# Optimization experiments

Measured on AMD Instinct MI355X. Metric: run time of the kernel, lower is better.

The kernel has to match this reference:

```python
import jax, jax.numpy as jnp
import numpy as np

N_LORAS = 8   # number of adapters (experts)
RANK = 16     # rank per adapter; rmoe = N_LORAS * RANK = 128
TEMP = 1.0    # self.T


def setup_inputs() -> dict:
    key = jax.random.key(0)
    ks = jax.random.split(key, 7)
    B, S, D_IN, D_OUT = 4, 2048, 4096, 4096
    RMOE = N_LORAS * RANK
    x = jax.random.normal(ks[0], (B, S, D_IN), dtype=jnp.float32)
    base_w = jax.random.normal(ks[1], (D_OUT, D_IN), dtype=jnp.float32) / np.sqrt(D_IN)
    base_b = jax.random.normal(ks[2], (D_OUT,), dtype=jnp.float32) * 0.01
    # nn.init.normal_(lora_A.weight, std=1/r); lora_B zero-init in torch, use small random here
    lora_A = jax.random.normal(ks[3], (RMOE, D_IN), dtype=jnp.float32) / RANK
    lora_B = jax.random.normal(ks[4], (D_OUT, RMOE), dtype=jnp.float32) * 0.02
    router_w = jax.random.normal(ks[5], (N_LORAS, D_IN), dtype=jnp.float32) / np.sqrt(D_IN)
    # scaling[name] = lora_alpha / sqrt(r) per adapter (use_rslora)
    scalings = jnp.full((N_LORAS,), 32.0 / np.sqrt(RANK), dtype=jnp.float32)
    return {"x": x, "base_w": base_w, "base_b": base_b, "lora_A": lora_A,
            "lora_B": lora_B, "router_w": router_w, "scalings": scalings, "top_k": 2}


def reference(x, base_w, base_b, lora_A, lora_B, router_w, scalings, top_k):
    # Base dense layer: y = x W^T + b
    base_out = jnp.einsum('bsd,od->bso', x, base_w) + base_b

    # Router: per-token logits over adapters, top-k, softmax over selected
    logits = jnp.einsum('bsd,ed->bse', x, router_w) / TEMP          # [B,S,E]
    topv, topi = jax.lax.top_k(logits, top_k)                        # [B,S,K]
    gate_k = jax.nn.softmax(topv, axis=-1)                           # [B,S,K]
    # dense per-expert gate: scatter top-k weights back to E slots
    gate_e = jnp.sum(jax.nn.one_hot(topi, N_LORAS, dtype=gate_k.dtype)
                     * gate_k[..., None], axis=-2)                   # [B,S,E]

    # Fused LoRA: h = x A^T over the concatenated rank dim, mask ranks by gate*scaling
    h = jnp.einsum('bsd,rd->bsr', x, lora_A)                         # [B,S,RMOE]
    rank_w = jnp.repeat(gate_e * scalings, RANK, axis=-1)            # [B,S,RMOE]
    lora_out = jnp.einsum('bsr,or->bso', h * rank_w, lora_B)         # [B,S,O]

    return base_out + lora_out
```

## Files before the change

### kernel.cpp

```cpp
#include <hip/hip_runtime.h>
#include <cstdint>

typedef unsigned short u16;
typedef float  f32x4 __attribute__((ext_vector_type(4)));
typedef short  s16x4 __attribute__((ext_vector_type(4)));
typedef short  s16x8 __attribute__((ext_vector_type(8)));

#define D_IN  4096
#define D_OUT 4096
#define RMOE  128
#define KAUG  4224
#define NTOK  8192

__device__ __forceinline__ u16 f2bf(float f) {
    unsigned u = __builtin_bit_cast(unsigned, f);
    unsigned r = u + 0x7fffu + ((u >> 16) & 1u);
    return (u16)(r >> 16);
}

__device__ __forceinline__ void gload16(const void* g, void* l) {
    __builtin_amdgcn_global_load_lds(
        (const __attribute__((address_space(1))) void*)g,
        (__attribute__((address_space(3))) void*)l, 16, 0, 0);
}

__global__ __launch_bounds__(256)
void xconv_router_kernel(const float* __restrict__ x, const float* __restrict__ rw,
                         const float* __restrict__ scal,
                         u16* __restrict__ Xaug, float* __restrict__ gates) {
    int wave = threadIdx.x >> 6, lane = threadIdx.x & 63;
    int t = blockIdx.x * 4 + wave;
    const float4* xp = (const float4*)(x + (long)t * D_IN);
    u16* xa = Xaug + (long)t * KAUG;
    float acc[8];
#pragma unroll
    for (int e = 0; e < 8; ++e) acc[e] = 0.f;
#pragma unroll 4
    for (int i = 0; i < 16; ++i) {
        float4 xv = xp[i * 64 + lane];
        s16x4 o;
        o[0] = (short)f2bf(xv.x); o[1] = (short)f2bf(xv.y);
        o[2] = (short)f2bf(xv.z); o[3] = (short)f2bf(xv.w);
        *(s16x4*)(xa + (i * 64 + lane) * 4) = o;
#pragma unroll
        for (int e = 0; e < 8; ++e) {
            float4 wv = ((const float4*)(rw + (long)e * D_IN))[i * 64 + lane];
            acc[e] += xv.x * wv.x + xv.y * wv.y + xv.z * wv.z + xv.w * wv.w;
        }
    }
#pragma unroll
    for (int e = 0; e < 8; ++e) {
#pragma unroll
        for (int off = 32; off > 0; off >>= 1)
            acc[e] += __shfl_xor(acc[e], off, 64);
    }
    if (lane == 0) {
        int i1 = 0; float v1 = acc[0];
#pragma unroll
        for (int e = 1; e < 8; ++e) if (acc[e] > v1) { v1 = acc[e]; i1 = e; }
        int i2 = -1; float v2 = -3.4e38f;
#pragma unroll
        for (int e = 0; e < 8; ++e) if (e != i1 && acc[e] > v2) { v2 = acc[e]; i2 = e; }
        float g1 = 1.f / (1.f + expf(v2 - v1));
        float g2 = 1.f - g1;
        float* gp = gates + (long)t * 8;
#pragma unroll
        for (int e = 0; e < 8; ++e)
            gp[e] = (e == i1) ? g1 * scal[e] : ((e == i2) ? g2 * scal[e] : 0.f);
    }
}

__global__ __launch_bounds__(256)
void convert_rest_kernel(const float* __restrict__ bw,
                         const float* __restrict__ lA, const float* __restrict__ lB,
                         u16* __restrict__ Waug, u16* __restrict__ A16) {
    const long nw = (long)D_OUT * D_IN / 8;
    const long nb = (long)D_OUT * RMOE / 8;
    long tid = (long)blockIdx.x * 256 + threadIdx.x;
    const float* src; u16* dst;
    if (tid < nw) {
        long e = tid * 8; long row = e >> 12; long col = e & 4095;
        src = bw + e; dst = Waug + row * KAUG + col;
    } else if (tid < nw + nb) {
        long e = (tid - nw) * 8; long row = e >> 7; long col = e & 127;
        src = lB + e; dst = Waug + row * KAUG + D_IN + col;
    } else {
        long e = (tid - nw - nb) * 8;
        src = lA + e; dst = A16 + e;
    }
    float4 a = ((const float4*)src)[0];
    float4 b = ((const float4*)src)[1];
    s16x8 o;
    o[0] = (short)f2bf(a.x); o[1] = (short)f2bf(a.y);
    o[2] = (short)f2bf(a.z); o[3] = (short)f2bf(a.w);
    o[4] = (short)f2bf(b.x); o[5] = (short)f2bf(b.y);
    o[6] = (short)f2bf(b.z); o[7] = (short)f2bf(b.w);
    *(s16x8*)dst = o;
}

__global__ __launch_bounds__(256)
void lora_h_kernel(u16* __restrict__ Xaug, const u16* __restrict__ A16,
                   const float* __restrict__ gates) {
    __shared__ u16 sX[64 * 32];
    __shared__ u16 sW[64 * 32];
    int tid = threadIdx.x, wave = tid >> 6, lane = tid & 63;
    int bm = blockIdx.x >> 1, bn = blockIdx.x & 1;
    long m0 = (long)bm * 64; int n0 = bn * 64;
    int wr = wave >> 1, wc = wave & 1;
    int c = wave * 64 + lane, row = c >> 2, oct = c & 3;
    const u16* gx = Xaug + (m0 + row) * KAUG + oct * 8;
    const u16* gw = A16 + (long)(n0 + row) * D_IN + oct * 8;
    u16* lx = sX + wave * 512;
    u16* lw = sW + wave * 512;
    int cl = lane & 15, kh = lane >> 4;
    int aoff[2], boff[2];
#pragma unroll
    for (int i = 0; i < 2; ++i) {
        aoff[i] = (wr * 32 + i * 16 + cl) * 32 + kh * 8;
        boff[i] = (wc * 32 + i * 16 + cl) * 32 + kh * 8;
    }
    f32x4 acc[2][2];
#pragma unroll
    for (int i = 0; i < 2; ++i)
#pragma unroll
        for (int j = 0; j < 2; ++j) acc[i][j] = (f32x4){0.f, 0.f, 0.f, 0.f};
    for (int kt = 0; kt < 128; ++kt) {
        __syncthreads();
        gload16(gx, lx); gload16(gw, lw);
        gx += 32; gw += 32;
        __syncthreads();
        s16x8 a[2], b[2];
#pragma unroll
        for (int i = 0; i < 2; ++i) {
            a[i] = *(const s16x8*)&sX[aoff[i]];
            b[i] = *(const s16x8*)&sW[boff[i]];
        }
#pragma unroll
        for (int mi = 0; mi < 2; ++mi)
#pragma unroll
            for (int ni = 0; ni < 2; ++ni)
                acc[mi][ni] = __builtin_amdgcn_mfma_f32_16x16x32_bf16(
                    a[mi], b[ni], acc[mi][ni], 0, 0, 0);
    }
#pragma unroll
    for (int ni = 0; ni < 2; ++ni) {
        int col = n0 + wc * 32 + ni * 16 + cl;
        int g = col >> 4;
#pragma unroll
        for (int mi = 0; mi < 2; ++mi) {
#pragma unroll
            for (int r = 0; r < 4; ++r) {
                long tok = m0 + wr * 32 + mi * 16 + kh * 4 + r;
                float v = acc[mi][ni][r] * gates[tok * 8 + g];
                Xaug[tok * KAUG + D_IN + col] = f2bf(v);
            }
        }
    }
}

__global__ __launch_bounds__(512, 2)
void main_gemm(const u16* __restrict__ Xaug, const u16* __restrict__ Waug,
               const float* __restrict__ bias, float* __restrict__ out) {
    __shared__ u16 lds[4 * 16384];
    const int tid = threadIdx.x;
    const int wave = tid >> 6, lane = tid & 63;
    const int cl = lane & 15, kh = lane >> 4;
    const int wr = wave >> 2, wc = wave & 3;

    int bid = blockIdx.x;
    int swz = (bid & 7) * 64 + (bid >> 3);
    long m0 = (long)(swz & 31) * 256;
    long n0 = (long)(swz >> 5) * 256;

    const int rA = tid >> 2;
    const int sl = (((tid & 3) ^ ((tid >> 3) & 3))) * 8;
    const u16* gA0 = Xaug + (m0 + rA) * KAUG + sl;
    const u16* gA1 = Xaug + (m0 + 128 + rA) * KAUG + sl;
    const u16* gB0 = Waug + (n0 + rA) * KAUG + sl;
    const u16* gB1 = Waug + (n0 + 128 + rA) * KAUG + sl;
    const int wbase = wave * 512;

    const int swk = (kh ^ ((cl >> 1) & 3)) * 8;
    const int aob = (wr * 128 + cl) * 32 + swk;
    const int bob = 8192 + (wc * 64 + cl) * 32 + swk;

    f32x4 acc[8][4];
#pragma unroll
    for (int m = 0; m < 8; ++m)
#pragma unroll
        for (int n = 0; n < 4; ++n) acc[m][n] = (f32x4){0.f, 0.f, 0.f, 0.f};

#define STAGE(t) do { u16* L = lds + ((t) & 3) * 16384 + wbase;              \
        gload16(gA0 + (t) * 32, L);                                          \
        gload16(gA1 + (t) * 32, L + 4096);                                   \
        gload16(gB0 + (t) * 32, L + 8192);                                   \
        gload16(gB1 + (t) * 32, L + 12288); } while (0)
#define READL(av, bv, Lb) do {                                               \
        _Pragma("unroll")                                                    \
        for (int m_ = 0; m_ < 8; ++m_)                                       \
            av[m_] = *(const s16x8*)&(Lb)[aob + m_ * 512];                   \
        _Pragma("unroll")                                                    \
        for (int n_ = 0; n_ < 4; ++n_)                                       \
            bv[n_] = *(const s16x8*)&(Lb)[bob + n_ * 512]; } while (0)
#define DOMFMA(av, bv) do {                                                  \
        __builtin_amdgcn_s_setprio(1);                                       \
        _Pragma("unroll")                                                    \
        for (int m_ = 0; m_ < 8; ++m_)                                       \
            _Pragma("unroll")                                                \
            for (int n_ = 0; n_ < 4; ++n_)                                   \
                acc[m_][n_] = __builtin_amdgcn_mfma_f32_16x16x32_bf16(       \
                    av[m_], bv[n_], acc[m_][n_], 0, 0, 0);                   \
        __builtin_amdgcn_s_setprio(0); } while (0)

    s16x8 av0[8], bv0[4], av1[8], bv1[4];

    STAGE(0); STAGE(1); STAGE(2);
    asm volatile("s_waitcnt vmcnt(8)" ::: "memory");
    __builtin_amdgcn_s_barrier();
    __builtin_amdgcn_sched_barrier(0);
    READL(av0, bv0, (lds + 0));

    for (int u = 0; u < 66; ++u) {
        const int tA = 2 * u, tB = 2 * u + 1;
        if (tA <= 128) asm volatile("s_waitcnt vmcnt(4)" ::: "memory");
        else           asm volatile("s_waitcnt vmcnt(0)" ::: "memory");
        __builtin_amdgcn_s_barrier();
        __builtin_amdgcn_sched_barrier(0);
        {
            const u16* Lb = lds + (tB & 3) * 16384;
            READL(av1, bv1, Lb);
            if (tA + 3 < 132) STAGE(tA + 3);
        }
        asm volatile("s_waitcnt lgkmcnt(12)" ::: "memory");
        __builtin_amdgcn_sched_barrier(0);
        DOMFMA(av0, bv0);
        if (tB < 131) {
            asm volatile("s_waitcnt vmcnt(4)" ::: "memory");
            __builtin_amdgcn_s_barrier();
            __builtin_amdgcn_sched_barrier(0);
            {
                const u16* Lb = lds + ((tB + 1) & 3) * 16384;
                READL(av0, bv0, Lb);
                if (tB + 3 < 132) STAGE(tB + 3);
            }
            asm volatile("s_waitcnt lgkmcnt(12)" ::: "memory");
            __builtin_amdgcn_sched_barrier(0);
        } else {
            asm volatile("s_waitcnt lgkmcnt(0)" ::: "memory");
            __builtin_amdgcn_sched_barrier(0);
        }
        DOMFMA(av1, bv1);
    }
#undef STAGE
#undef READL
#undef DOMFMA

#pragma unroll
    for (int n = 0; n < 4; ++n) {
        long col = n0 + wc * 64 + n * 16 + cl;
        float bvv = bias[col];
#pragma unroll
        for (int m = 0; m < 8; ++m) {
            long row = m0 + wr * 128 + m * 16 + kh * 4;
#pragma unroll
            for (int r = 0; r < 4; ++r)
                out[(row + r) * (long)D_OUT + col] = acc[m][n][r] + bvv;
        }
    }
}

extern "C" void kernel_launch(void* const* d_in, const int* in_sizes, int n_in,
                              void* d_out, int out_size, void* d_ws, size_t ws_size,
                              hipStream_t stream) {
    const float* x  = (const float*)d_in[0];
    const float* bw = (const float*)d_in[1];
    const float* bb = (const float*)d_in[2];
    const float* lA = (const float*)d_in[3];
    const float* lB = (const float*)d_in[4];
    const float* rw = (const float*)d_in[5];
    const float* sc = (const float*)d_in[6];
    float* out = (float*)d_out;

    char* ws = (char*)d_ws;
    u16* Xaug  = (u16*)ws;
    u16* Waug  = (u16*)(ws + 69206016);
    u16* A16   = (u16*)(ws + 103809024);
    float* gates = (float*)(ws + 104857600);

    xconv_router_kernel<<<2048, 256, 0, stream>>>(x, rw, sc, Xaug, gates);
    convert_rest_kernel<<<8704, 256, 0, stream>>>(bw, lA, lB, Waug, A16);
    lora_h_kernel<<<256, 256, 0, stream>>>(Xaug, A16, gates);
    main_gemm<<<512, 512, 0, stream>>>(Xaug, Waug, bb, out);
}
```

Measured before the change: 402.0 us.

## Merge prep kernels into one launch and split lora_h into more blocks

```diff
diff --git a/kernel.cpp b/kernel.cpp
--- a/kernel.cpp
+++ b/kernel.cpp
@@ -25,135 +25,125 @@
 }
 
 __global__ __launch_bounds__(256)
-void xconv_router_kernel(const float* __restrict__ x, const float* __restrict__ rw,
-                         const float* __restrict__ scal,
-                         u16* __restrict__ Xaug, float* __restrict__ gates) {
-    int wave = threadIdx.x >> 6, lane = threadIdx.x & 63;
-    int t = blockIdx.x * 4 + wave;
-    const float4* xp = (const float4*)(x + (long)t * D_IN);
-    u16* xa = Xaug + (long)t * KAUG;
-    float acc[8];
-#pragma unroll
-    for (int e = 0; e < 8; ++e) acc[e] = 0.f;
+void prep_kernel(const float* __restrict__ x, const float* __restrict__ rw,
+                 const float* __restrict__ scal, const float* __restrict__ bw,
+                 const float* __restrict__ lA, const float* __restrict__ lB,
+                 u16* __restrict__ Xaug, u16* __restrict__ Waug,
+                 u16* __restrict__ A16, float* __restrict__ gates) {
+    if (blockIdx.x < 2048) {
+        int wave = threadIdx.x >> 6, lane = threadIdx.x & 63;
+        int t = blockIdx.x * 4 + wave;
+        const float4* xp = (const float4*)(x + (long)t * D_IN);
+        u16* xa = Xaug + (long)t * KAUG;
+        float acc[8];
+#pragma unroll
+        for (int e = 0; e < 8; ++e) acc[e] = 0.f;
 #pragma unroll 4
-    for (int i = 0; i < 16; ++i) {
-        float4 xv = xp[i * 64 + lane];
-        s16x4 o;
-        o[0] = (short)f2bf(xv.x); o[1] = (short)f2bf(xv.y);
-        o[2] = (short)f2bf(xv.z); o[3] = (short)f2bf(xv.w);
-        *(s16x4*)(xa + (i * 64 + lane) * 4) = o;
+        for (int i = 0; i < 16; ++i) {
+            float4 xv = xp[i * 64 + lane];
+            s16x4 o;
+            o[0] = (short)f2bf(xv.x); o[1] = (short)f2bf(xv.y);
+            o[2] = (short)f2bf(xv.z); o[3] = (short)f2bf(xv.w);
+            *(s16x4*)(xa + (i * 64 + lane) * 4) = o;
+#pragma unroll
+            for (int e = 0; e < 8; ++e) {
+                float4 wv = ((const float4*)(rw + (long)e * D_IN))[i * 64 + lane];
+                acc[e] += xv.x * wv.x + xv.y * wv.y + xv.z * wv.z + xv.w * wv.w;
+            }
+        }
 #pragma unroll
         for (int e = 0; e < 8; ++e) {
-            float4 wv = ((const float4*)(rw + (long)e * D_IN))[i * 64 + lane];
-            acc[e] += xv.x * wv.x + xv.y * wv.y + xv.z * wv.z + xv.w * wv.w;
-        }
-    }
-#pragma unroll
-    for (int e = 0; e < 8; ++e) {
-#pragma unroll
-        for (int off = 32; off > 0; off >>= 1)
-            acc[e] += __shfl_xor(acc[e], off, 64);
-    }
-    if (lane == 0) {
-        int i1 = 0; float v1 = acc[0];
-#pragma unroll
-        for (int e = 1; e < 8; ++e) if (acc[e] > v1) { v1 = acc[e]; i1 = e; }
-        int i2 = -1; float v2 = -3.4e38f;
-#pragma unroll
-        for (int e = 0; e < 8; ++e) if (e != i1 && acc[e] > v2) { v2 = acc[e]; i2 = e; }
-        float g1 = 1.f / (1.f + expf(v2 - v1));
-        float g2 = 1.f - g1;
-        float* gp = gates + (long)t * 8;
-#pragma unroll
-        for (int e = 0; e < 8; ++e)
-            gp[e] = (e == i1) ? g1 * scal[e] : ((e == i2) ? g2 * scal[e] : 0.f);
-    }
-}
-
-__global__ __launch_bounds__(256)
-void convert_rest_kernel(const float* __restrict__ bw,
-                         const float* __restrict__ lA, const float* __restrict__ lB,
-                         u16* __restrict__ Waug, u16* __restrict__ A16) {
-    const long nw = (long)D_OUT * D_IN / 8;
-    const long nb = (long)D_OUT * RMOE / 8;
-    long tid = (long)blockIdx.x * 256 + threadIdx.x;
-    const float* src; u16* dst;
-    if (tid < nw) {
-        long e = tid * 8; long row = e >> 12; long col = e & 4095;
-        src = bw + e; dst = Waug + row * KAUG + col;
-    } else if (tid < nw + nb) {
-        long e = (tid - nw) * 8; long row = e >> 7; long col = e & 127;
-        src = lB + e; dst = Waug + row * KAUG + D_IN + col;
+#pragma unroll
+            for (int off = 32; off > 0; off >>= 1)
+                acc[e] += __shfl_xor(acc[e], off, 64);
+        }
+        if (lane == 0) {
+            int i1 = 0; float v1 = acc[0];
+#pragma unroll
+            for (int e = 1; e < 8; ++e) if (acc[e] > v1) { v1 = acc[e]; i1 = e; }
+            int i2 = -1; float v2 = -3.4e38f;
+#pragma unroll
+            for (int e = 0; e < 8; ++e) if (e != i1 && acc[e] > v2) { v2 = acc[e]; i2 = e; }
+            float g1 = 1.f / (1.f + expf(v2 - v1));
+            float g2 = 1.f - g1;
+            float* gp = gates + (long)t * 8;
+#pragma unroll
+            for (int e = 0; e < 8; ++e)
+                gp[e] = (e == i1) ? g1 * scal[e] : ((e == i2) ? g2 * scal[e] : 0.f);
+        }
     } else {
-        long e = (tid - nw - nb) * 8;
-        src = lA + e; dst = A16 + e;
-    }
-    float4 a = ((const float4*)src)[0];
-    float4 b = ((const float4*)src)[1];
-    s16x8 o;
-    o[0] = (short)f2bf(a.x); o[1] = (short)f2bf(a.y);
-    o[2] = (short)f2bf(a.z); o[3] = (short)f2bf(a.w);
-    o[4] = (short)f2bf(b.x); o[5] = (short)f2bf(b.y);
-    o[6] = (short)f2bf(b.z); o[7] = (short)f2bf(b.w);
-    *(s16x8*)dst = o;
+        const long nw = (long)D_OUT * D_IN / 8;
+        const long nb = (long)D_OUT * RMOE / 8;
+        long tid = (long)(blockIdx.x - 2048) * 256 + threadIdx.x;
+        const float* src; u16* dst;
+        if (tid < nw) {
+            long e = tid * 8; long row = e >> 12; long col = e & 4095;
+            src = bw + e; dst = Waug + row * KAUG + col;
+        } else if (tid < nw + nb) {
+            long e = (tid - nw) * 8; long row = e >> 7; long col = e & 127;
+            src = lB + e; dst = Waug + row * KAUG + D_IN + col;
+        } else {
+            long e = (tid - nw - nb) * 8;
+            src = lA + e; dst = A16 + e;
+        }
+        float4 a = ((const float4*)src)[0];
+        float4 b = ((const float4*)src)[1];
+        s16x8 o;
+        o[0] = (short)f2bf(a.x); o[1] = (short)f2bf(a.y);
+        o[2] = (short)f2bf(a.z); o[3] = (short)f2bf(a.w);
+        o[4] = (short)f2bf(b.x); o[5] = (short)f2bf(b.y);
+        o[6] = (short)f2bf(b.z); o[7] = (short)f2bf(b.w);
+        *(s16x8*)dst = o;
+    }
 }
 
 __global__ __launch_bounds__(256)
 void lora_h_kernel(u16* __restrict__ Xaug, const u16* __restrict__ A16,
                    const float* __restrict__ gates) {
     __shared__ u16 sX[64 * 32];
-    __shared__ u16 sW[64 * 32];
+    __shared__ u16 sW[32 * 32];
     int tid = threadIdx.x, wave = tid >> 6, lane = tid & 63;
-    int bm = blockIdx.x >> 1, bn = blockIdx.x & 1;
-    long m0 = (long)bm * 64; int n0 = bn * 64;
+    int bm = blockIdx.x >> 2, bn = blockIdx.x & 3;
+    long m0 = (long)bm * 64; int n0 = bn * 32;
     int wr = wave >> 1, wc = wave & 1;
-    int c = wave * 64 + lane, row = c >> 2, oct = c & 3;
-    const u16* gx = Xaug + (m0 + row) * KAUG + oct * 8;
-    const u16* gw = A16 + (long)(n0 + row) * D_IN + oct * 8;
+    int rowA = tid >> 2, oct = tid & 3;
+    const u16* gx = Xaug + (m0 + rowA) * KAUG + oct * 8;
+    const u16* gw = A16 + (long)(n0 + rowA) * D_IN + oct * 8;
     u16* lx = sX + wave * 512;
     u16* lw = sW + wave * 512;
     int cl = lane & 15, kh = lane >> 4;
-    int aoff[2], boff[2];
-#pragma unroll
-    for (int i = 0; i < 2; ++i) {
+    int aoff[2];
+#pragma unroll
+    for (int i = 0; i < 2; ++i)
         aoff[i] = (wr * 32 + i * 16 + cl) * 32 + kh * 8;
-        boff[i] = (wc * 32 + i * 16 + cl) * 32 + kh * 8;
-    }
-    f32x4 acc[2][2];
-#pragma unroll
-    for (int i = 0; i < 2; ++i)
-#pragma unroll
-        for (int j = 0; j < 2; ++j) acc[i][j] = (f32x4){0.f, 0.f, 0.f, 0.f};
+    int boff = (wc * 16 + cl) * 32 + kh * 8;
+    f32x4 acc2[2];
+    acc2[0] = (f32x4){0.f, 0.f, 0.f, 0.f};
+    acc2[1] = (f32x4){0.f, 0.f, 0.f, 0.f};
     for (int kt = 0; kt < 128; ++kt) {
         __syncthreads();
-        gload16(gx, lx); gload16(gw, lw);
+        gload16(gx, lx);
+        if (tid < 128) gload16(gw, lw);
         gx += 32; gw += 32;
         __syncthreads();
-        s16x8 a[2], b[2];
-#pragma unroll
-        for (int i = 0; i < 2; ++i) {
-            a[i] = *(const s16x8*)&sX[aoff[i]];
-            b[i] = *(const s16x8*)&sW[boff[i]];
-        }
+        s16x8 a[2], b;
+        a[0] = *(const s16x8*)&sX[aoff[0]];
+        a[1] = *(const s16x8*)&sX[aoff[1]];
+        b = *(const s16x8*)&sW[boff];
 #pragma unroll
         for (int mi = 0; mi < 2; ++mi)
-#pragma unroll
-            for (int ni = 0; ni < 2; ++ni)
-                acc[mi][ni] = __builtin_amdgcn_mfma_f32_16x16x32_bf16(
-                    a[mi], b[ni], acc[mi][ni], 0, 0, 0);
-    }
-#pragma unroll
-    for (int ni = 0; ni < 2; ++ni) {
-        int col = n0 + wc * 32 + ni * 16 + cl;
-        int g = col >> 4;
-#pragma unroll
-        for (int mi = 0; mi < 2; ++mi) {
-#pragma unroll
-            for (int r = 0; r < 4; ++r) {
-                long tok = m0 + wr * 32 + mi * 16 + kh * 4 + r;
-                float v = acc[mi][ni][r] * gates[tok * 8 + g];
-                Xaug[tok * KAUG + D_IN + col] = f2bf(v);
-            }
+            acc2[mi] = __builtin_amdgcn_mfma_f32_16x16x32_bf16(
+                a[mi], b, acc2[mi], 0, 0, 0);
+    }
+    int col = n0 + wc * 16 + cl;
+    int g = col >> 4;
+#pragma unroll
+    for (int mi = 0; mi < 2; ++mi) {
+#pragma unroll
+        for (int r = 0; r < 4; ++r) {
+            long tok = m0 + wr * 32 + mi * 16 + kh * 4 + r;
+            float v = acc2[mi][r] * gates[tok * 8 + g];
+            Xaug[tok * KAUG + D_IN + col] = f2bf(v);
         }
     }
 }
@@ -287,8 +277,8 @@
     u16* A16   = (u16*)(ws + 103809024);
     float* gates = (float*)(ws + 104857600);
 
-    xconv_router_kernel<<<2048, 256, 0, stream>>>(x, rw, sc, Xaug, gates);
-    convert_rest_kernel<<<8704, 256, 0, stream>>>(bw, lA, lB, Waug, A16);
-    lora_h_kernel<<<256, 256, 0, stream>>>(Xaug, A16, gates);
+    prep_kernel<<<10752, 256, 0, stream>>>(x, rw, sc, bw, lA, lB,
+                                           Xaug, Waug, A16, gates);
+    lora_h_kernel<<<512, 256, 0, stream>>>(Xaug, A16, gates);
     main_gemm<<<512, 512, 0, stream>>>(Xaug, Waug, bb, out);
 }
```

Result: faster. 388.3 us (-3.4%).
